# Performance work log

Measured on AMD Instinct MI355X. Metric: run time of the kernel, lower is better.

Reference implementation:

```python
import jax, jax.numpy as jnp
import numpy as np

B, DV, W, H = 128, 2048, 14, 14
S = W * H            # 196 spatial positions
DQ = 2048            # question vector dim
DA = 1200            # attention dim_v == dim_q == dim_mm (MLB elementwise fusion)
G = 4                # nb_glimpses
DH = 2048            # fusion dim_h (total); per-glimpse = DH // G
NANS = 3000


def setup_inputs() -> dict:
    key = jax.random.key(0)
    ks = jax.random.split(key, 16)
    s = 0.02
    return {
        "input_v": jax.random.normal(ks[0], (B, DV, W, H), jnp.float32),
        "x_q_vec": jax.random.normal(ks[1], (B, DQ), jnp.float32),
        # conv_v_att: 1x1 conv DV->DA  (expressed as channel matmul)
        "Wv_att": jax.random.normal(ks[2], (DV, DA), jnp.float32) * s,
        "bv_att": jnp.zeros((DA,), jnp.float32),
        # linear_q_att: DQ->DA
        "Wq_att": jax.random.normal(ks[3], (DQ, DA), jnp.float32) * s,
        "bq_att": jnp.zeros((DA,), jnp.float32),
        # conv_att: 1x1 conv DA->G
        "Wa": jax.random.normal(ks[4], (DA, G), jnp.float32) * s,
        "ba": jnp.zeros((G,), jnp.float32),
        # per-glimpse fusion linears DV -> DH//G, stacked over glimpses
        "Wf": jax.random.normal(ks[5], (G, DV, DH // G), jnp.float32) * s,
        "bf": jnp.zeros((G, DH // G), jnp.float32),
        # linear_q_fusion: DQ -> DH
        "Wqf": jax.random.normal(ks[6], (DQ, DH), jnp.float32) * s,
        "bqf": jnp.zeros((DH,), jnp.float32),
        # linear_classif: DH -> NANS
        "Wc": jax.random.normal(ks[7], (DH, NANS), jnp.float32) * s,
        "bc": jnp.zeros((NANS,), jnp.float32),
    }


def reference(input_v, x_q_vec, Wv_att, bv_att, Wq_att, bq_att, Wa, ba,
              Wf, bf, Wqf, bqf, Wc, bc):
    b = input_v.shape[0]
    v_flat = input_v.reshape(b, DV, S)                      # [B, DV, S]

    # --- attention scores ---
    # conv_v_att (1x1) + tanh -> [B, S, DA]
    x_v = jnp.tanh(jnp.einsum('bcs,cd->bsd', v_flat, Wv_att) + bv_att)
    # linear_q_att + tanh -> [B, DA], broadcast over spatial
    x_q = jnp.tanh(x_q_vec @ Wq_att + bq_att)
    # MLB fusion_att: elementwise multiply, then tanh (activation_mm)
    x_att = jnp.tanh(x_v * x_q[:, None, :])                 # [B, S, DA]
    scores = jnp.einsum('bsd,dg->bsg', x_att, Wa) + ba      # [B, S, G]
    att = jax.nn.softmax(scores, axis=1)                    # softmax over spatial

    # --- weighted pooling per glimpse ---
    v_att = jnp.einsum('bsg,bcs->bgc', att, v_flat)         # [B, G, DV]

    # --- fusion of glimpses ---
    xv = jnp.tanh(jnp.einsum('bgc,gch->bgh', v_att, Wf) + bf)  # [B, G, DH/G]
    xv = xv.reshape(b, DH)                                   # concat glimpses
    xq = jnp.tanh(x_q_vec @ Wqf + bqf)                       # [B, DH]
    x = xv * xq                                              # MLB fusion_classif

    # --- classifier ---
    x = jnp.tanh(x)
    return x @ Wc + bc                                       # [B, NANS]
```

## Files before the change

### kernel.cpp

```cpp
#include <hip/hip_runtime.h>
#include <hip/hip_bf16.h>

#define BB   128
#define DV   2048
#define SS   196
#define DQ   2048
#define DA   1200
#define DAP  1280
#define GG   4
#define DH   2048
#define NANS 3000
#define NANSP 3008
#define MROWS (BB*SS)
#define NT   5
#define KSPLIT 8
#define KCHUNK (DV/KSPLIT)
#define NQ   (DAP + DH)

typedef __attribute__((ext_vector_type(8))) short bf16x8;
typedef __attribute__((ext_vector_type(4))) float f32x4;

__device__ __forceinline__ float fast_tanh(float x) {
    float e = __expf(2.0f * x);
    return 1.0f - 2.0f * __builtin_amdgcn_rcpf(e + 1.0f);
}

__device__ __forceinline__ void async_copy16(const void* gsrc, void* ldst) {
    __builtin_amdgcn_global_load_lds(
        (const __attribute__((address_space(1))) void*)gsrc,
        (__attribute__((address_space(3))) void*)ldst, 16, 0, 0);
}

__global__ void pad_misc(const float* __restrict__ bv, const float* __restrict__ Wa,
                         float* __restrict__ bvp, float* __restrict__ wap) {
    int i = blockIdx.x * 256 + threadIdx.x;
    if (i < DAP) bvp[i] = (i < DA) ? bv[i] : 0.f;
    if (i < DAP * GG) {
        int d = i >> 2;
        wap[i] = (d < DA) ? Wa[i] : 0.f;
    }
}

__global__ __launch_bounds__(256) void transpose_v(const float* __restrict__ v,
                                                   __hip_bfloat16* __restrict__ vt) {
    const int b    = blockIdx.z;
    const int t    = threadIdx.x;
    const int lane = t & 63;
    const int w    = t >> 6;
    const int sl   = lane >> 2;
    const int cq   = lane & 3;
    const int s    = blockIdx.y * 16 + sl;
    const int c0   = blockIdx.x * 128 + w * 32 + cq * 8;
    if (s >= SS) return;
    const float* src = v + (size_t)b * DV * SS + (size_t)c0 * SS + s;
    float f[8];
#pragma unroll
    for (int i = 0; i < 8; ++i) f[i] = src[(size_t)i * SS];
    union { bf16x8 v8; __hip_bfloat16 h[8]; } u;
#pragma unroll
    for (int i = 0; i < 8; ++i) u.h[i] = __float2bfloat16(f[i]);
    *(bf16x8*)(vt + ((size_t)b * SS + s) * DV + c0) = u.v8;
}

__global__ __launch_bounds__(256) void transpose_w(const float* __restrict__ Wv,
                                                   __hip_bfloat16* __restrict__ wvt) {
    __shared__ float tile[64][65];
    const int d0 = blockIdx.x * 64;
    const int c0 = blockIdx.y * 64;
    const int t  = threadIdx.x;
    const int col  = t & 63;
    const int rowb = t >> 6;
#pragma unroll
    for (int i = 0; i < 16; ++i) {
        int c = rowb + i * 4;
        int d = d0 + col;
        tile[c][col] = (d < DA) ? Wv[(size_t)(c0 + c) * DA + d] : 0.f;
    }
    __syncthreads();
#pragma unroll
    for (int i = 0; i < 16; ++i) {
        int dl = rowb + i * 4;
        wvt[(size_t)(d0 + dl) * DV + c0 + col] = __float2bfloat16(tile[col][dl]);
    }
}

template <int SEL>
__global__ __launch_bounds__(256) void gemm_partial(
    const float* __restrict__ A, int lda,
    const float* __restrict__ Bm, const float* __restrict__ B2,
    float* __restrict__ Cp, int Npad) {
    __shared__ float As[64 * 132];
    __shared__ float Bs[64 * 68];
    const int t     = threadIdx.x;
    const int n0    = blockIdx.x * 64;
    const int kbase = blockIdx.y * KCHUNK;

    const float* Aeff = A;
    const float* Beff;
    int ldb, ncol0, nlim;
    if (SEL == 0) {
        Beff = Bm; ldb = NANS; ncol0 = n0; nlim = NANS;
    } else if (SEL == 1) {
        int gg = n0 >> 9;
        Aeff = A + gg * 2048;
        Beff = Bm + (size_t)gg * 2048 * 512;
        ldb = 512; ncol0 = n0 & 511; nlim = 1 << 30;
    } else {
        if (n0 < DAP) { Beff = Bm; ldb = DA; ncol0 = n0;      nlim = DA; }
        else          { Beff = B2; ldb = DH; ncol0 = n0 - DAP; nlim = 1 << 30; }
    }

    const int tm = (t & 31) * 4;
    const int tn = (t >> 5) * 8;
    float acc[4][8] = {};

    for (int k0 = kbase; k0 < kbase + KCHUNK; k0 += 64) {
        {
            int kk = t & 63, mb = (t >> 6) * 32;
#pragma unroll
            for (int i = 0; i < 32; ++i)
                As[kk * 132 + mb + i] = Aeff[(size_t)(mb + i) * lda + k0 + kk];
        }
        {
            int j = t & 63, kr = t >> 6;
            bool ok = (ncol0 + j) < nlim;
#pragma unroll
            for (int i = 0; i < 16; ++i) {
                int k = kr + i * 4;
                Bs[k * 68 + j] = ok ? Beff[(size_t)(k0 + k) * ldb + ncol0 + j] : 0.f;
            }
        }
        __syncthreads();
#pragma unroll
        for (int kk = 0; kk < 64; ++kk) {
            const float4 av = *(const float4*)(As + kk * 132 + tm);
            const float4 b0 = *(const float4*)(Bs + kk * 68 + tn);
            const float4 b1 = *(const float4*)(Bs + kk * 68 + tn + 4);
            const float am[4] = {av.x, av.y, av.z, av.w};
#pragma unroll
            for (int i = 0; i < 4; ++i) {
                acc[i][0] += am[i] * b0.x; acc[i][1] += am[i] * b0.y;
                acc[i][2] += am[i] * b0.z; acc[i][3] += am[i] * b0.w;
                acc[i][4] += am[i] * b1.x; acc[i][5] += am[i] * b1.y;
                acc[i][6] += am[i] * b1.z; acc[i][7] += am[i] * b1.w;
            }
        }
        __syncthreads();
    }
#pragma unroll
    for (int i = 0; i < 4; ++i) {
        size_t base = ((size_t)blockIdx.y * 128 + tm + i) * Npad + n0 + tn;
        float4 v0 = {acc[i][0], acc[i][1], acc[i][2], acc[i][3]};
        float4 v1 = {acc[i][4], acc[i][5], acc[i][6], acc[i][7]};
        *(float4*)(Cp + base) = v0;
        *(float4*)(Cp + base + 4) = v1;
    }
}

template <int MODE>
__global__ __launch_bounds__(256) void gemm_epilogue(
    const float* __restrict__ Cp, int Npad, int Nreal,
    const float* __restrict__ bias, const float* __restrict__ aux,
    float* __restrict__ out, int ldo) {
    int n = blockIdx.x * 256 + threadIdx.x;
    int m = blockIdx.y;
    if (n >= Npad) return;
    float s = 0.f;
#pragma unroll
    for (int ks = 0; ks < KSPLIT; ++ks)
        s += Cp[((size_t)ks * 128 + m) * Npad + n];
    if (MODE == 0) {
        if (n >= Nreal) return;
        out[(size_t)m * ldo + n] = s + bias[n];
    } else {
        float xv = fast_tanh(s + bias[n]);
        out[(size_t)m * ldo + n] = fast_tanh(xv * aux[(size_t)m * 2048 + n]);
    }
}

__global__ __launch_bounds__(256) void epilogue_q(
    const float* __restrict__ Cp,
    const float* __restrict__ bqa, const float* __restrict__ bqf,
    float* __restrict__ qatt, float* __restrict__ qfus) {
    int n = blockIdx.x * 256 + threadIdx.x;
    int m = blockIdx.y;
    if (n >= NQ) return;
    float s = 0.f;
#pragma unroll
    for (int ks = 0; ks < KSPLIT; ++ks)
        s += Cp[((size_t)ks * 128 + m) * NQ + n];
    if (n < DAP) {
        qatt[(size_t)m * DAP + n] = (n < DA) ? fast_tanh(s + bqa[n]) : 0.f;
    } else {
        int j = n - DAP;
        qfus[(size_t)m * DH + j] = fast_tanh(s + bqf[j]);
    }
}

__global__ __launch_bounds__(512, 2) void big_gemm(
    const __hip_bfloat16* __restrict__ vt,
    const __hip_bfloat16* __restrict__ wt,
    const float* __restrict__ bvp,
    const float* __restrict__ qatt,
    const float* __restrict__ wap,
    float* __restrict__ scores_p) {
    __shared__ __align__(16) char lds[131072];
    __shared__ __align__(16) float wa_s[256 * 4];
    __shared__ float qs[3 * 256];

    const int t    = threadIdx.x;
    const int lane = t & 63;
    const int w    = t >> 6;
    const int wr   = w >> 2;
    const int wc   = w & 3;

    int bid = blockIdx.x;
    int grp = bid / 40, r = bid % 40;
    int mt, nt;
    if (grp < 12) { mt = grp * 8 + (r & 7); nt = r >> 3; }
    else          { mt = 96 + (r & 1);      nt = r >> 1; }
    const int m0 = mt * 256, n0 = nt * 256;
    const int b_lo = m0 / SS;
    const int bs1  = (b_lo + 1) * SS;
    const int bs2  = (b_lo + 2) * SS;

    if (t < 256) *(float4*)(wa_s + t * 4) = *(const float4*)(wap + (n0 + t) * 4);
    {
        int j = t >> 8, c = t & 255;
        int b = b_lo + j;
        qs[t] = (b < BB) ? qatt[(size_t)b * DAP + n0 + c] : 0.f;
        if (t < 256) {
            int b2 = b_lo + 2;
            qs[512 + t] = (b2 < BB) ? qatt[(size_t)b2 * DAP + n0 + t] : 0.f;
        }
    }
    __syncthreads();

    const int srow   = t >> 2;
    const int schunk = (t & 3) ^ ((t >> 3) & 3);
    const __hip_bfloat16* aG = vt + (size_t)(m0 + srow) * DV + schunk * 8;
    const __hip_bfloat16* bG = wt + (size_t)(n0 + srow) * DV + schunk * 8;

    auto STAGE_ITEM = [&](int buf, int k, int p) {
        const int ks = p >> 1, mat = p & 1;
        const __hip_bfloat16* g = (mat ? bG : aG) + (size_t)k * 64 + ks * 32;
        char* dst = lds + buf * 65536 + ks * 32768 + mat * 16384 + t * 16;
        async_copy16(g, dst);
        async_copy16(g + (size_t)128 * DV, dst + 8192);
    };

    const int rchk = ((lane >> 4) ^ (((lane & 15) >> 1) & 3)) * 16;
    const int aRow = (wr * 128 + (lane & 15)) * 64;
    const int bRow = (wc * 64 + (lane & 15)) * 64;

    f32x4 acc[8][4];
#pragma unroll
    for (int i = 0; i < 8; ++i)
#pragma unroll
        for (int j = 0; j < 4; ++j) acc[i][j] = (f32x4){0.f, 0.f, 0.f, 0.f};

    STAGE_ITEM(0, 0, 0); STAGE_ITEM(0, 0, 1);
    STAGE_ITEM(0, 0, 2); STAGE_ITEM(0, 0, 3);
    asm volatile("s_waitcnt vmcnt(4)" ::: "memory");
    __builtin_amdgcn_s_barrier();

    for (int kt = 0; kt < 32; ++kt) {
        const int cur = kt & 1;
        const char* Xb = lds + cur * 65536;
#pragma unroll
        for (int ks = 0; ks < 2; ++ks) {
            const char* Ar = Xb + ks * 32768;
            if (kt < 31) {
                STAGE_ITEM(cur ^ 1, kt + 1, 2 * ks);
                STAGE_ITEM(cur ^ 1, kt + 1, 2 * ks + 1);
            }
            bf16x8 bfr[4], afr[4];
#pragma unroll
            for (int ni = 0; ni < 4; ++ni)
                bfr[ni] = *(const bf16x8*)(Ar + 16384 + bRow + (ni * 16) * 64 + rchk);
#pragma unroll
            for (int q = 0; q < 4; ++q)
                afr[q] = *(const bf16x8*)(Ar + aRow + (q * 16) * 64 + rchk);
            __builtin_amdgcn_s_setprio(1);
#pragma unroll
            for (int q = 0; q < 4; ++q)
#pragma unroll
                for (int ni = 0; ni < 4; ++ni)
                    acc[q][ni] = __builtin_amdgcn_mfma_f32_16x16x32_bf16(
                        afr[q], bfr[ni], acc[q][ni], 0, 0, 0);
            __builtin_amdgcn_s_setprio(0);
            __builtin_amdgcn_sched_barrier(0x8);
            bf16x8 af2[4];
#pragma unroll
            for (int q = 0; q < 4; ++q)
                af2[q] = *(const bf16x8*)(Ar + aRow + ((4 + q) * 16) * 64 + rchk);
            __builtin_amdgcn_s_setprio(1);
#pragma unroll
            for (int q = 0; q < 4; ++q)
#pragma unroll
                for (int ni = 0; ni < 4; ++ni)
                    acc[4 + q][ni] = __builtin_amdgcn_mfma_f32_16x16x32_bf16(
                        af2[q], bfr[ni], acc[4 + q][ni], 0, 0, 0);
            __builtin_amdgcn_s_setprio(0);
            if (kt < 31) asm volatile("s_waitcnt vmcnt(4)" ::: "memory");
            else         asm volatile("s_waitcnt vmcnt(0)" ::: "memory");
            __builtin_amdgcn_s_barrier();
        }
    }

    __syncthreads();
    float* sc = (float*)lds;

    const int colb_l = wc * 64 + (lane & 15);
    const int colb_g = n0 + colb_l;
    float bvv[4];
    float4 wv[4];
#pragma unroll
    for (int ni = 0; ni < 4; ++ni) {
        bvv[ni] = bvp[colb_g + ni * 16];
        wv[ni]  = *(const float4*)(wa_s + (colb_l + ni * 16) * 4);
    }
#pragma unroll
    for (int mi = 0; mi < 8; ++mi) {
#pragma unroll
        for (int rr = 0; rr < 4; ++rr) {
            int lrow = wr * 128 + mi * 16 + ((lane >> 4) << 2) + rr;
            int row  = m0 + lrow;
            int qoff = (row >= bs1 ? 256 : 0) + (row >= bs2 ? 256 : 0);
            float p0 = 0.f, p1 = 0.f, p2 = 0.f, p3 = 0.f;
#pragma unroll
            for (int ni = 0; ni < 4; ++ni) {
                float xv = fast_tanh(acc[mi][ni][rr] + bvv[ni]);
                float xa = fast_tanh(xv * qs[qoff + colb_l + ni * 16]);
                p0 += xa * wv[ni].x; p1 += xa * wv[ni].y;
                p2 += xa * wv[ni].z; p3 += xa * wv[ni].w;
            }
#pragma unroll
            for (int mk = 1; mk < 16; mk <<= 1) {
                p0 += __shfl_xor(p0, mk); p1 += __shfl_xor(p1, mk);
                p2 += __shfl_xor(p2, mk); p3 += __shfl_xor(p3, mk);
            }
            if ((lane & 15) == 0)
                *(float4*)(sc + ((size_t)wc * 256 + lrow) * 4) =
                    (float4){p0, p1, p2, p3};
        }
    }
    __syncthreads();
    if (t < 256) {
        float4 s0 = *(float4*)(sc + (0 * 256 + t) * 4);
        float4 s1 = *(float4*)(sc + (1 * 256 + t) * 4);
        float4 s2 = *(float4*)(sc + (2 * 256 + t) * 4);
        float4 s3 = *(float4*)(sc + (3 * 256 + t) * 4);
        float4 s = {s0.x + s1.x + s2.x + s3.x, s0.y + s1.y + s2.y + s3.y,
                    s0.z + s1.z + s2.z + s3.z, s0.w + s1.w + s2.w + s3.w};
        *(float4*)(scores_p + ((size_t)nt * MROWS + m0 + t) * 4) = s;
    }
}

__global__ __launch_bounds__(256) void softmax_pool(
    const float* __restrict__ scores_p,
    const __hip_bfloat16* __restrict__ vt,
    float* __restrict__ vatt) {
    __shared__ __align__(16) float att[SS * GG];
    const int b = blockIdx.y;
    const int t = threadIdx.x;
    if (t < SS) {
        float4 s = {0.f, 0.f, 0.f, 0.f};
#pragma unroll
        for (int ntile = 0; ntile < NT; ++ntile) {
            float4 p = *(const float4*)(scores_p + ((size_t)ntile * MROWS + b * SS + t) * 4);
            s.x += p.x; s.y += p.y; s.z += p.z; s.w += p.w;
        }
        *(float4*)(att + t * 4) = s;
    }
    __syncthreads();
    {
        const int g = t >> 6;
        const int lane = t & 63;
        float mx = -3.0e38f;
        for (int s = lane; s < SS; s += 64) mx = fmaxf(mx, att[s * 4 + g]);
#pragma unroll
        for (int m = 32; m > 0; m >>= 1) mx = fmaxf(mx, __shfl_xor(mx, m));
        float sum = 0.f;
        for (int s = lane; s < SS; s += 64) sum += __expf(att[s * 4 + g] - mx);
#pragma unroll
        for (int m = 32; m > 0; m >>= 1) sum += __shfl_xor(sum, m);
        float inv = __builtin_amdgcn_rcpf(sum);
        for (int s = lane; s < SS; s += 64) att[s * 4 + g] = __expf(att[s * 4 + g] - mx) * inv;
    }
    __syncthreads();
    const int c = blockIdx.x * 1024 + t * 4;
    const __hip_bfloat16* vp = vt + (size_t)b * SS * DV + c;
    float a0[4] = {}, a1[4] = {}, a2[4] = {}, a3[4] = {};
#pragma unroll 4
    for (int s = 0; s < SS; ++s) {
        uint2 u = *(const uint2*)(vp + (size_t)s * DV);
        float v0 = __uint_as_float(u.x << 16);
        float v1 = __uint_as_float(u.x & 0xffff0000u);
        float v2 = __uint_as_float(u.y << 16);
        float v3 = __uint_as_float(u.y & 0xffff0000u);
        float4 aw = *(const float4*)(att + s * 4);
        a0[0] += v0 * aw.x; a0[1] += v0 * aw.y; a0[2] += v0 * aw.z; a0[3] += v0 * aw.w;
        a1[0] += v1 * aw.x; a1[1] += v1 * aw.y; a1[2] += v1 * aw.z; a1[3] += v1 * aw.w;
        a2[0] += v2 * aw.x; a2[1] += v2 * aw.y; a2[2] += v2 * aw.z; a2[3] += v2 * aw.w;
        a3[0] += v3 * aw.x; a3[1] += v3 * aw.y; a3[2] += v3 * aw.z; a3[3] += v3 * aw.w;
    }
    float* vb = vatt + (size_t)b * GG * DV;
#pragma unroll
    for (int g = 0; g < GG; ++g) {
        float4 o = {a0[g], a1[g], a2[g], a3[g]};
        *(float4*)(vb + (size_t)g * DV + c) = o;
    }
}

extern "C" void kernel_launch(void* const* d_in, const int* in_sizes, int n_in,
                              void* d_out, int out_size, void* d_ws, size_t ws_size,
                              hipStream_t stream) {
    const float* input_v = (const float*)d_in[0];
    const float* x_q     = (const float*)d_in[1];
    const float* Wv      = (const float*)d_in[2];
    const float* bv      = (const float*)d_in[3];
    const float* Wq_att  = (const float*)d_in[4];
    const float* bq_att  = (const float*)d_in[5];
    const float* Wa      = (const float*)d_in[6];
    const float* Wf      = (const float*)d_in[8];
    const float* bf_     = (const float*)d_in[9];
    const float* Wqf     = (const float*)d_in[10];
    const float* bqf     = (const float*)d_in[11];
    const float* Wc      = (const float*)d_in[12];
    const float* bc      = (const float*)d_in[13];
    float* out = (float*)d_out;

    char* wsb = (char*)d_ws;
    size_t off = 0;
    auto carve = [&](size_t bytes) -> void* {
        void* p = wsb + off;
        off += (bytes + 255) & ~(size_t)255;
        return p;
    };
    __hip_bfloat16* vt  = (__hip_bfloat16*)carve((size_t)MROWS * DV * 2);
    __hip_bfloat16* wvt = (__hip_bfloat16*)carve((size_t)DAP * DV * 2);
    float* Cp       = (float*)carve((size_t)KSPLIT * 128 * NQ * 4);
    float* scores_p = (float*)carve((size_t)NT * MROWS * GG * 4);
    float* qatt = (float*)carve((size_t)BB * DAP * 4);
    float* qfus = (float*)carve((size_t)BB * DH * 4);
    float* bvp  = (float*)carve((size_t)DAP * 4);
    float* wap  = (float*)carve((size_t)DAP * GG * 4);
    float* vatt = (float*)carve((size_t)BB * GG * DV * 4);
    float* xbuf = (float*)carve((size_t)BB * DH * 4);
    (void)ws_size; (void)n_in; (void)in_sizes; (void)out_size;

    pad_misc<<<dim3(20), 256, 0, stream>>>(bv, Wa, bvp, wap);
    transpose_v<<<dim3(DV / 128, 13, BB), 256, 0, stream>>>(input_v, vt);
    transpose_w<<<dim3(DAP / 64, DV / 64), 256, 0, stream>>>(Wv, wvt);

    gemm_partial<2><<<dim3(NQ / 64, KSPLIT), 256, 0, stream>>>(
        x_q, DQ, Wq_att, Wqf, Cp, NQ);
    epilogue_q<<<dim3(NQ / 256, BB), 256, 0, stream>>>(Cp, bq_att, bqf, qatt, qfus);

    big_gemm<<<dim3(490), 512, 0, stream>>>(vt, wvt, bvp, qatt, wap, scores_p);

    softmax_pool<<<dim3(2, BB), 256, 0, stream>>>(scores_p, vt, vatt);

    gemm_partial<1><<<dim3(DH / 64, KSPLIT), 256, 0, stream>>>(
        vatt, GG * DV, Wf, nullptr, Cp, DH);
    gemm_epilogue<2><<<dim3(DH / 256, BB), 256, 0, stream>>>(
        Cp, DH, DH, bf_, qfus, xbuf, DH);

    gemm_partial<0><<<dim3(NANSP / 64, KSPLIT), 256, 0, stream>>>(
        xbuf, DH, Wc, nullptr, Cp, NANSP);
    gemm_epilogue<0><<<dim3(NANSP / 256 + 1, BB), 256, 0, stream>>>(
        Cp, NANSP, NANS, bc, nullptr, out, NANS);
}
```

Measured before the change: 672.3 us.

## Deepen async-copy pipeline with finer-grained staging and barriers per phase

Restructures the main GEMM k-loop into four phases per k-tile, each issuing one staged async copy, and prefetches the first item of tile k+2 so more global loads are in flight. The per-phase waitcnt and barrier keep more outstanding loads while computing. It adds a barrier per phase, which could raise synchronisation cost, and the LDS buffer reuse timing becomes more delicate.

Result: faster. 642.4 us (-4.4%).

```diff
diff --git a/kernel.cpp b/kernel.cpp
--- a/kernel.cpp
+++ b/kernel.cpp
@@ -241,10 +241,10 @@
     const __hip_bfloat16* aG = vt + (size_t)(m0 + srow) * DV + schunk * 8;
     const __hip_bfloat16* bG = wt + (size_t)(n0 + srow) * DV + schunk * 8;
 
-    auto STAGE_ITEM = [&](int buf, int k, int p) {
+    auto STAGE_ITEM = [&](int k, int p) {
         const int ks = p >> 1, mat = p & 1;
         const __hip_bfloat16* g = (mat ? bG : aG) + (size_t)k * 64 + ks * 32;
-        char* dst = lds + buf * 65536 + ks * 32768 + mat * 16384 + t * 16;
+        char* dst = lds + (k & 1) * 65536 + ks * 32768 + mat * 16384 + t * 16;
         async_copy16(g, dst);
         async_copy16(g + (size_t)128 * DV, dst + 8192);
     };
@@ -259,52 +259,51 @@
 #pragma unroll
         for (int j = 0; j < 4; ++j) acc[i][j] = (f32x4){0.f, 0.f, 0.f, 0.f};
 
-    STAGE_ITEM(0, 0, 0); STAGE_ITEM(0, 0, 1);
-    STAGE_ITEM(0, 0, 2); STAGE_ITEM(0, 0, 3);
-    asm volatile("s_waitcnt vmcnt(4)" ::: "memory");
+    STAGE_ITEM(0, 0); STAGE_ITEM(0, 1);
+    STAGE_ITEM(0, 2); STAGE_ITEM(0, 3);
+    STAGE_ITEM(1, 0);
+    asm volatile("s_waitcnt vmcnt(6)" ::: "memory");
     __builtin_amdgcn_s_barrier();
 
     for (int kt = 0; kt < 32; ++kt) {
         const int cur = kt & 1;
         const char* Xb = lds + cur * 65536;
-#pragma unroll
-        for (int ks = 0; ks < 2; ++ks) {
+        bf16x8 bfr[4];
+#pragma unroll
+        for (int p = 0; p < 4; ++p) {
+            const int ks = p >> 1, mh = p & 1;
             const char* Ar = Xb + ks * 32768;
-            if (kt < 31) {
-                STAGE_ITEM(cur ^ 1, kt + 1, 2 * ks);
-                STAGE_ITEM(cur ^ 1, kt + 1, 2 * ks + 1);
-            }
-            bf16x8 bfr[4], afr[4];
-#pragma unroll
-            for (int ni = 0; ni < 4; ++ni)
-                bfr[ni] = *(const bf16x8*)(Ar + 16384 + bRow + (ni * 16) * 64 + rchk);
+            bf16x8 afr[4];
 #pragma unroll
             for (int q = 0; q < 4; ++q)
-                afr[q] = *(const bf16x8*)(Ar + aRow + (q * 16) * 64 + rchk);
+                afr[q] = *(const bf16x8*)(Ar + aRow + (mh * 64 + q * 16) * 64 + rchk);
+            if (mh == 0) {
+#pragma unroll
+                for (int ni = 0; ni < 4; ++ni)
+                    bfr[ni] = *(const bf16x8*)(Ar + 16384 + bRow + (ni * 16) * 64 + rchk);
+            }
+            if (p < 3) {
+                if (kt < 31) STAGE_ITEM(kt + 1, p + 1);
+            } else {
+                if (kt < 30) STAGE_ITEM(kt + 2, 0);
+            }
+            if (p == 1) {
+                if (kt < 31) asm volatile("s_waitcnt vmcnt(6)" ::: "memory");
+                else         asm volatile("s_waitcnt vmcnt(0)" ::: "memory");
+            } else if (p == 3) {
+                if (kt < 30)       asm volatile("s_waitcnt vmcnt(6)" ::: "memory");
+                else if (kt == 30) asm volatile("s_waitcnt vmcnt(4)" ::: "memory");
+                else               asm volatile("s_waitcnt vmcnt(0)" ::: "memory");
+            }
+            __builtin_amdgcn_s_barrier();
             __builtin_amdgcn_s_setprio(1);
 #pragma unroll
             for (int q = 0; q < 4; ++q)
 #pragma unroll
                 for (int ni = 0; ni < 4; ++ni)
-                    acc[q][ni] = __builtin_amdgcn_mfma_f32_16x16x32_bf16(
-                        afr[q], bfr[ni], acc[q][ni], 0, 0, 0);
+                    acc[mh * 4 + q][ni] = __builtin_amdgcn_mfma_f32_16x16x32_bf16(
+                        afr[q], bfr[ni], acc[mh * 4 + q][ni], 0, 0, 0);
             __builtin_amdgcn_s_setprio(0);
-            __builtin_amdgcn_sched_barrier(0x8);
-            bf16x8 af2[4];
-#pragma unroll
-            for (int q = 0; q < 4; ++q)
-                af2[q] = *(const bf16x8*)(Ar + aRow + ((4 + q) * 16) * 64 + rchk);
-            __builtin_amdgcn_s_setprio(1);
-#pragma unroll
-            for (int q = 0; q < 4; ++q)
-#pragma unroll
-                for (int ni = 0; ni < 4; ++ni)
-                    acc[4 + q][ni] = __builtin_amdgcn_mfma_f32_16x16x32_bf16(
-                        af2[q], bfr[ni], acc[4 + q][ni], 0, 0, 0);
-            __builtin_amdgcn_s_setprio(0);
-            if (kt < 31) asm volatile("s_waitcnt vmcnt(4)" ::: "memory");
-            else         asm volatile("s_waitcnt vmcnt(0)" ::: "memory");
-            __builtin_amdgcn_s_barrier();
         }
     }
 
```
